# Kernel optimization log

Hardware: AMD Instinct MI355X
Metric: run time of the kernel (lower is better)

Reference implementation:

```python
import jax, jax.numpy as jnp
import numpy as np

B, N, M = 64, 1024, 80
C1, D = 288, 256  # object_dim, lang_dim
EPS = 1e-12  # F.normalize eps


def setup_inputs() -> dict:
    key = jax.random.key(0)
    ks = jax.random.split(key, 16)
    w = lambda k, s: jax.random.normal(k, s, jnp.float32) * 0.05
    object_feat = jax.random.normal(ks[0], (B, N, C1), jnp.float32)
    lang_feat = jax.random.normal(ks[1], (B, M, D), jnp.float32)
    lang_mask = jax.random.randint(ks[2], (B, M), 0, 2).astype(jnp.int32)
    lang_mask = lang_mask.at[:, 0].set(1)  # ensure >=1 valid token per row
    return {
        "object_feat": object_feat,
        "lang_feat": lang_feat,
        "lang_mask": lang_mask,
        # object_att_fc: Linear(C1,D) -> ReLU -> Linear(D,D)
        "W1": w(ks[3], (C1, D)), "b1": w(ks[4], (D,)),
        "W2": w(ks[5], (D, D)), "b2": w(ks[6], (D,)),
        # atten_fc: Dropout(eval=identity) -> Linear(2D,1)
        "Wa": w(ks[7], (2 * D, 1)), "ba": w(ks[8], (1,)),
        # object_score_fc: Linear(C1,D) -> ReLU -> Linear(D,D)
        "W3": w(ks[9], (C1, D)), "b3": w(ks[10], (D,)),
        "W4": w(ks[11], (D, D)), "b4": w(ks[12], (D,)),
        # score_fc: Dropout(eval=identity) -> Linear(D,1)
        "Ws": w(ks[13], (D, 1)), "bs": w(ks[14], (1,)),
    }


def reference(object_feat, lang_feat, lang_mask, W1, b1, W2, b2, Wa, ba, W3, b3, W4, b4, Ws, bs):
    # object attention features: (B,N,D)
    oa = jnp.maximum(object_feat @ W1 + b1, 0.0) @ W2 + b2
    # additive attention: cat([oa, lang]) @ Wa == oa @ Wa[:D] + lang @ Wa[D:]
    w_o, w_l = Wa[:D, 0], Wa[D:, 0]
    score = (oa @ w_o)[:, :, None] + (lang_feat @ w_l)[:, None, :] + ba[0]  # (B,N,M)
    score = jnp.where(lang_mask[:, None, :] == 0, -jnp.inf, score)
    att = jax.nn.softmax(score, axis=2)  # (B,N,M)
    att_feat = jnp.einsum("bnm,bmd->bnd", att, lang_feat)  # sum(att * lang_att)
    # object score branch
    osc = jnp.maximum(object_feat @ W3 + b3, 0.0) @ W4 + b4  # (B,N,D)
    x = jnp.maximum(att_feat * osc, 0.0)
    # F.normalize over channel dim (dim=2)
    nrm = jnp.sqrt(jnp.sum(x * x, axis=2, keepdims=True))
    x = x / jnp.maximum(nrm, EPS)
    out = x @ Ws + bs  # (B,N,1)
    return jnp.transpose(out, (0, 2, 1))  # (B,1,N)
```

## Files before the change

### kernel.cpp

```cpp
#include <hip/hip_runtime.h>
#include <math.h>
#include <stdint.h>

#define B_  64
#define N_  1024
#define M_  80
#define C1_ 288
#define D_  256
#define EPS_ 1e-12f

typedef _Float16 f16;
typedef _Float16 f16x8 __attribute__((ext_vector_type(8)));
typedef _Float16 f16x4 __attribute__((ext_vector_type(4)));
typedef float    f32x4 __attribute__((ext_vector_type(4)));

#define ATT_OFF 0
#define W3F_OFF 65536
#define W4F_OFF (65536 + 147456)

__global__ __launch_bounds__(256) void prep_kernel(
    const float* __restrict__ lang_feat,
    const int*   __restrict__ lang_mask,
    const float* __restrict__ Wa,
    float* __restrict__ att_ws)
{
    __shared__ float wl_s[D_];
    __shared__ float ls[M_];
    const int b   = blockIdx.x;
    const int tid = threadIdx.x;

    wl_s[tid] = Wa[D_ + tid];
    __syncthreads();

    const int wave = tid >> 6, lane = tid & 63;
    for (int m = wave; m < M_; m += 4) {
        const float* lf = lang_feat + (size_t)(b * M_ + m) * D_;
        float p = 0.f;
        #pragma unroll
        for (int j = 0; j < 4; ++j) { int d = lane + 64 * j; p = fmaf(lf[d], wl_s[d], p); }
        #pragma unroll
        for (int off = 32; off; off >>= 1) p += __shfl_xor(p, off);
        if (lane == 0) ls[m] = (lang_mask[b * M_ + m] == 0) ? -INFINITY : p;
    }
    __syncthreads();

    float mx = -INFINITY;
    for (int m = 0; m < M_; ++m) mx = fmaxf(mx, ls[m]);
    __syncthreads();
    if (tid < M_) ls[tid] = expf(ls[tid] - mx);
    __syncthreads();

    float sm = 0.f;
    for (int m = 0; m < M_; ++m) sm += ls[m];

    const int d = tid;
    float acc = 0.f;
    for (int m = 0; m < M_; ++m)
        acc = fmaf(ls[m], lang_feat[(size_t)(b * M_ + m) * D_ + d], acc);
    att_ws[b * D_ + d] = acc / sm;
}

__global__ __launch_bounds__(256) void wprep_kernel(
    const float* __restrict__ W3, const float* __restrict__ W4,
    f16* __restrict__ w3f, f16* __restrict__ w4f)
{
    const int kb = blockIdx.x;
    const float* src; f16* dst; int K0;
    if (kb < 9) { src = W3; dst = w3f + kb * 8192;      K0 = kb * 32; }
    else        { src = W4; dst = w4f + (kb - 9) * 8192; K0 = (kb - 9) * 32; }
    for (int idx = threadIdx.x; idx < 8192; idx += 256) {
        int nt  = idx >> 9;
        int rem = idx & 511;
        int ln  = rem >> 3;
        int i   = rem & 7;
        int k   = K0 + ((ln >> 4) << 3) + i;
        int col = (nt << 4) + (ln & 15);
        dst[idx] = (f16)src[k * D_ + col];
    }
}

__device__ __forceinline__ void g2l16(const void* g, void* l) {
    __builtin_amdgcn_global_load_lds(
        (const __attribute__((address_space(1))) uint32_t*)g,
        (__attribute__((address_space(3))) uint32_t*)l, 16, 0, 0);
}

#define ABYTES 36864
#define BBUF   16384

__global__ __launch_bounds__(512) void main_kernel(
    const float* __restrict__ obj,
    const f16*  __restrict__ w3f,
    const f16*  __restrict__ w4f,
    const float* __restrict__ b3,
    const float* __restrict__ b4,
    const float* __restrict__ Ws,
    const float* __restrict__ bs,
    const float* __restrict__ att,
    float* __restrict__ out)
{
    extern __shared__ char smem[];
    char* Areg = smem;
    char* Breg = smem + ABYTES;

    const int tid  = threadIdx.x;
    const int lane = tid & 63;
    const int w    = tid >> 6;
    const int mt   = w & 3;
    const int ng   = w >> 2;
    const int r0   = blockIdx.x * 64;
    const int b    = blockIdx.x >> 4;

    {
        const float4* src = (const float4*)(obj + (size_t)r0 * C1_);
        for (int idx = tid; idx < 64 * 72; idx += 512) {
            int row = idx / 72;
            int c   = (idx - row * 72) * 4;
            float4 v = src[idx];
            int plane = (row >> 4) * 9 + (c >> 5);
            int lane2 = (row & 15) + (((c & 31) >> 3) << 4);
            int ii    = c & 7;
            f16x4 h = { (f16)v.x, (f16)v.y, (f16)v.z, (f16)v.w };
            *(f16x4*)&Areg[plane * 1024 + lane2 * 16 + ii * 2] = h;
        }
    }

    const int colbase = (ng << 7) + (lane & 15);

    f32x4 acc[8];
    #pragma unroll
    for (int nt = 0; nt < 8; ++nt) {
        float bv = b3[colbase + (nt << 4)];
        acc[nt] = (f32x4){bv, bv, bv, bv};
    }

    {
        const char* g = (const char*)w3f + (w * 2) * 1024 + lane * 16;
        char* l = Breg + (w * 2) * 1024;
        g2l16(g, l); g2l16(g + 1024, l + 1024);
    }
    __syncthreads();

    for (int ks = 0; ks < 9; ++ks) {
        if (ks < 8) {
            const char* g = (const char*)w3f + (ks + 1) * BBUF + (w * 2) * 1024 + lane * 16;
            char* l = Breg + ((ks + 1) & 1) * BBUF + (w * 2) * 1024;
            g2l16(g, l); g2l16(g + 1024, l + 1024);
        }
        f16x8 a = *(const f16x8*)&Areg[(mt * 9 + ks) * 1024 + lane * 16];
        const char* bb = Breg + (ks & 1) * BBUF + (ng << 13);
        #pragma unroll
        for (int nt = 0; nt < 8; ++nt) {
            f16x8 bf = *(const f16x8*)&bb[nt * 1024 + lane * 16];
            acc[nt] = __builtin_amdgcn_mfma_f32_16x16x32_f16(a, bf, acc[nt], 0, 0, 0);
        }
        __syncthreads();
    }

    #pragma unroll
    for (int nt = 0; nt < 8; ++nt) {
        int colg  = colbase + (nt << 4);
        int plane = (mt << 3) + (colg >> 5);
        int l2b   = (((colg & 31) >> 3) << 4);
        int i2    = colg & 7;
        #pragma unroll
        for (int r = 0; r < 4; ++r) {
            int row_l = ((lane >> 4) << 2) + r;
            *(f16*)&Areg[plane * 1024 + (l2b + row_l) * 16 + i2 * 2] = (f16)fmaxf(acc[nt][r], 0.f);
        }
    }

    #pragma unroll
    for (int nt = 0; nt < 8; ++nt) {
        float bv = b4[colbase + (nt << 4)];
        acc[nt] = (f32x4){bv, bv, bv, bv};
    }
    {
        const char* g = (const char*)w4f + (w * 2) * 1024 + lane * 16;
        char* l = Breg + (w * 2) * 1024;
        g2l16(g, l); g2l16(g + 1024, l + 1024);
    }
    __syncthreads();

    for (int ks = 0; ks < 8; ++ks) {
        if (ks < 7) {
            const char* g = (const char*)w4f + (ks + 1) * BBUF + (w * 2) * 1024 + lane * 16;
            char* l = Breg + ((ks + 1) & 1) * BBUF + (w * 2) * 1024;
            g2l16(g, l); g2l16(g + 1024, l + 1024);
        }
        f16x8 a = *(const f16x8*)&Areg[(mt * 8 + ks) * 1024 + lane * 16];
        const char* bb = Breg + (ks & 1) * BBUF + (ng << 13);
        #pragma unroll
        for (int nt = 0; nt < 8; ++nt) {
            f16x8 bf = *(const f16x8*)&bb[nt * 1024 + lane * 16];
            acc[nt] = __builtin_amdgcn_mfma_f32_16x16x32_f16(a, bf, acc[nt], 0, 0, 0);
        }
        __syncthreads();
    }

    const float bsv = bs[0];
    float s2r[4] = {0, 0, 0, 0}, swr[4] = {0, 0, 0, 0};
    #pragma unroll
    for (int nt = 0; nt < 8; ++nt) {
        int colg = colbase + (nt << 4);
        float av = att[(b << 8) + colg];
        float wv = Ws[colg];
        #pragma unroll
        for (int r = 0; r < 4; ++r) {
            float x = fmaxf(av * acc[nt][r], 0.f);
            s2r[r] = fmaf(x, x, s2r[r]);
            swr[r] = fmaf(x, wv, swr[r]);
        }
    }
    #pragma unroll
    for (int off = 1; off < 16; off <<= 1) {
        #pragma unroll
        for (int r = 0; r < 4; ++r) {
            s2r[r] += __shfl_xor(s2r[r], off);
            swr[r] += __shfl_xor(swr[r], off);
        }
    }
    float* red = (float*)Breg;
    if (ng == 0 && (lane & 15) == 0) {
        #pragma unroll
        for (int r = 0; r < 4; ++r) {
            int row = (mt << 4) + ((lane >> 4) << 2) + r;
            red[row * 2]     = s2r[r];
            red[row * 2 + 1] = swr[r];
        }
    }
    __syncthreads();
    if (ng == 1 && (lane & 15) == 0) {
        #pragma unroll
        for (int r = 0; r < 4; ++r) {
            int row = (mt << 4) + ((lane >> 4) << 2) + r;
            float S2 = s2r[r] + red[row * 2];
            float SW = swr[r] + red[row * 2 + 1];
            out[r0 + row] = SW / fmaxf(sqrtf(S2), EPS_) + bsv;
        }
    }
}

extern "C" void kernel_launch(void* const* d_in, const int* in_sizes, int n_in,
                              void* d_out, int out_size, void* d_ws, size_t ws_size,
                              hipStream_t stream) {
    const float* object_feat = (const float*)d_in[0];
    const float* lang_feat   = (const float*)d_in[1];
    const int*   lang_mask   = (const int*)d_in[2];
    const float* Wa = (const float*)d_in[7];
    const float* W3 = (const float*)d_in[9];
    const float* b3 = (const float*)d_in[10];
    const float* W4 = (const float*)d_in[11];
    const float* b4 = (const float*)d_in[12];
    const float* Ws = (const float*)d_in[13];
    const float* bs = (const float*)d_in[14];
    float* out = (float*)d_out;

    char* ws  = (char*)d_ws;
    float* att = (float*)(ws + ATT_OFF);
    f16*  w3f = (f16*)(ws + W3F_OFF);
    f16*  w4f = (f16*)(ws + W4F_OFF);

    prep_kernel<<<B_, 256, 0, stream>>>(lang_feat, lang_mask, Wa, att);
    wprep_kernel<<<17, 256, 0, stream>>>(W3, W4, w3f, w4f);

    main_kernel<<<(B_ * N_) / 64, 512, ABYTES + 2 * BBUF, stream>>>(
        object_feat, w3f, w4f, b3, b4, Ws, bs, att, out);
}
```

Measured before the change: 173.9 us.

## Split fused MLP into two weight-resident GEMM kernels with f16 intermediate

Replaces the single fused kernel, which streamed weights through double-buffered LDS per 64-row tile, with two kernels. Each kernel loads the whole f16 weight matrix into LDS once per block, and each wave computes 32 rows by 256 columns straight from global A loads. The hidden activation h3 is written to workspace as f16, and the two prep kernels are merged into one launch. The cost is an extra global round trip for h3, very large LDS use (144KB and 128KB) that limits occupancy, and heavy register pressure from 32 accumulators per wave.

```diff
diff --git a/kernel.cpp b/kernel.cpp
--- a/kernel.cpp
+++ b/kernel.cpp
@@ -11,22 +11,49 @@
 
 typedef _Float16 f16;
 typedef _Float16 f16x8 __attribute__((ext_vector_type(8)));
-typedef _Float16 f16x4 __attribute__((ext_vector_type(4)));
 typedef float    f32x4 __attribute__((ext_vector_type(4)));
 
 #define ATT_OFF 0
 #define W3F_OFF 65536
 #define W4F_OFF (65536 + 147456)
+#define H3_OFF  (65536 + 147456 + 131072)
+
+__device__ __forceinline__ void g2l16(const void* g, void* l) {
+    __builtin_amdgcn_global_load_lds(
+        (const __attribute__((address_space(1))) uint32_t*)g,
+        (__attribute__((address_space(3))) uint32_t*)l, 16, 0, 0);
+}
 
 __global__ __launch_bounds__(256) void prep_kernel(
     const float* __restrict__ lang_feat,
     const int*   __restrict__ lang_mask,
     const float* __restrict__ Wa,
-    float* __restrict__ att_ws)
+    const float* __restrict__ W3,
+    const float* __restrict__ W4,
+    float* __restrict__ att_ws,
+    f16* __restrict__ w3f, f16* __restrict__ w4f)
 {
+    const int bi = blockIdx.x;
+    if (bi >= B_) {
+        const int kb = bi - B_;
+        const float* src; f16* dst; int K0;
+        if (kb < 9) { src = W3; dst = w3f + kb * 8192;       K0 = kb * 32; }
+        else        { src = W4; dst = w4f + (kb - 9) * 8192; K0 = (kb - 9) * 32; }
+        for (int idx = threadIdx.x; idx < 8192; idx += 256) {
+            int nt  = idx >> 9;
+            int rem = idx & 511;
+            int ln  = rem >> 3;
+            int i   = rem & 7;
+            int k   = K0 + ((ln >> 4) << 3) + i;
+            int col = (nt << 4) + (ln & 15);
+            dst[idx] = (f16)src[k * D_ + col];
+        }
+        return;
+    }
+
     __shared__ float wl_s[D_];
     __shared__ float ls[M_];
-    const int b   = blockIdx.x;
+    const int b   = bi;
     const int tid = threadIdx.x;
 
     wl_s[tid] = Wa[D_ + tid];
@@ -45,54 +72,111 @@
     __syncthreads();
 
     float mx = -INFINITY;
-    for (int m = 0; m < M_; ++m) mx = fmaxf(mx, ls[m]);
+    #pragma unroll
+    for (int m0 = 0; m0 < M_; m0 += 8) {
+        float v0 = ls[m0], v1 = ls[m0+1], v2 = ls[m0+2], v3 = ls[m0+3];
+        float v4 = ls[m0+4], v5 = ls[m0+5], v6 = ls[m0+6], v7 = ls[m0+7];
+        mx = fmaxf(mx, fmaxf(fmaxf(fmaxf(v0,v1), fmaxf(v2,v3)),
+                             fmaxf(fmaxf(v4,v5), fmaxf(v6,v7))));
+    }
     __syncthreads();
     if (tid < M_) ls[tid] = expf(ls[tid] - mx);
     __syncthreads();
 
-    float sm = 0.f;
-    for (int m = 0; m < M_; ++m) sm += ls[m];
+    float s0 = 0.f, s1 = 0.f, s2 = 0.f, s3 = 0.f;
+    #pragma unroll
+    for (int m0 = 0; m0 < M_; m0 += 8) {
+        s0 += ls[m0] + ls[m0+4];
+        s1 += ls[m0+1] + ls[m0+5];
+        s2 += ls[m0+2] + ls[m0+6];
+        s3 += ls[m0+3] + ls[m0+7];
+    }
+    const float inv = 1.f / ((s0 + s1) + (s2 + s3));
 
     const int d = tid;
-    float acc = 0.f;
-    for (int m = 0; m < M_; ++m)
-        acc = fmaf(ls[m], lang_feat[(size_t)(b * M_ + m) * D_ + d], acc);
-    att_ws[b * D_ + d] = acc / sm;
-}
-
-__global__ __launch_bounds__(256) void wprep_kernel(
-    const float* __restrict__ W3, const float* __restrict__ W4,
-    f16* __restrict__ w3f, f16* __restrict__ w4f)
-{
-    const int kb = blockIdx.x;
-    const float* src; f16* dst; int K0;
-    if (kb < 9) { src = W3; dst = w3f + kb * 8192;      K0 = kb * 32; }
-    else        { src = W4; dst = w4f + (kb - 9) * 8192; K0 = (kb - 9) * 32; }
-    for (int idx = threadIdx.x; idx < 8192; idx += 256) {
-        int nt  = idx >> 9;
-        int rem = idx & 511;
-        int ln  = rem >> 3;
-        int i   = rem & 7;
-        int k   = K0 + ((ln >> 4) << 3) + i;
-        int col = (nt << 4) + (ln & 15);
-        dst[idx] = (f16)src[k * D_ + col];
-    }
-}
-
-__device__ __forceinline__ void g2l16(const void* g, void* l) {
-    __builtin_amdgcn_global_load_lds(
-        (const __attribute__((address_space(1))) uint32_t*)g,
-        (__attribute__((address_space(3))) uint32_t*)l, 16, 0, 0);
-}
-
-#define ABYTES 36864
-#define BBUF   16384
-
-__global__ __launch_bounds__(512) void main_kernel(
+    float a0 = 0.f, a1 = 0.f, a2 = 0.f, a3 = 0.f;
+    const float* lfb = lang_feat + (size_t)b * M_ * D_ + d;
+    #pragma unroll 5
+    for (int m = 0; m < M_; m += 4) {
+        a0 = fmaf(ls[m],   lfb[(size_t)m * D_],       a0);
+        a1 = fmaf(ls[m+1], lfb[(size_t)(m+1) * D_],   a1);
+        a2 = fmaf(ls[m+2], lfb[(size_t)(m+2) * D_],   a2);
+        a3 = fmaf(ls[m+3], lfb[(size_t)(m+3) * D_],   a3);
+    }
+    att_ws[b * D_ + d] = ((a0 + a1) + (a2 + a3)) * inv;
+}
+
+__global__ __launch_bounds__(512, 2) void gemm1_kernel(
     const float* __restrict__ obj,
     const f16*  __restrict__ w3f,
+    const float* __restrict__ b3,
+    f16* __restrict__ h3)
+{
+    extern __shared__ char smem[];
+    const int tid  = threadIdx.x;
+    const int lane = tid & 63;
+    const int w    = tid >> 6;
+
+    #pragma unroll
+    for (int i = 0; i < 18; ++i) {
+        int off = (i * 512 + tid) * 16;
+        g2l16((const char*)w3f + off, smem + off);
+    }
+    __syncthreads();
+
+    const int r0   = (blockIdx.x * 8 + w) * 32;
+    const int colc = lane & 15;
+    const int kc   = (lane >> 4) << 3;
+
+    f32x4 acc0[16], acc1[16];
+    #pragma unroll
+    for (int nt = 0; nt < 16; ++nt) {
+        float bv = b3[(nt << 4) + colc];
+        acc0[nt] = (f32x4){bv, bv, bv, bv};
+        acc1[nt] = acc0[nt];
+    }
+
+    const float* arow0 = obj + (size_t)(r0 + colc) * C1_ + kc;
+    const float* arow1 = arow0 + 16 * C1_;
+
+    #pragma unroll 3
+    for (int ks = 0; ks < 9; ++ks) {
+        float4 p00 = *(const float4*)(arow0 + ks * 32);
+        float4 p01 = *(const float4*)(arow0 + ks * 32 + 4);
+        float4 p10 = *(const float4*)(arow1 + ks * 32);
+        float4 p11 = *(const float4*)(arow1 + ks * 32 + 4);
+        f16x8 a0 = {(f16)p00.x,(f16)p00.y,(f16)p00.z,(f16)p00.w,
+                    (f16)p01.x,(f16)p01.y,(f16)p01.z,(f16)p01.w};
+        f16x8 a1 = {(f16)p10.x,(f16)p10.y,(f16)p10.z,(f16)p10.w,
+                    (f16)p11.x,(f16)p11.y,(f16)p11.z,(f16)p11.w};
+        const char* bb = smem + ks * 16384;
+        #pragma unroll
+        for (int nt = 0; nt < 16; ++nt) {
+            f16x8 bf = *(const f16x8*)&bb[nt * 1024 + lane * 16];
+            acc0[nt] = __builtin_amdgcn_mfma_f32_16x16x32_f16(a0, bf, acc0[nt], 0, 0, 0);
+            acc1[nt] = __builtin_amdgcn_mfma_f32_16x16x32_f16(a1, bf, acc1[nt], 0, 0, 0);
+        }
+    }
+
+    const int rbase = (lane >> 4) << 2;
+    #pragma unroll
+    for (int h = 0; h < 2; ++h) {
+        #pragma unroll
+        for (int r = 0; r < 4; ++r) {
+            int row = r0 + 16 * h + rbase + r;
+            f16* dst = h3 + (size_t)row * D_ + colc;
+            #pragma unroll
+            for (int nt = 0; nt < 16; ++nt) {
+                f32x4 a = h ? acc1[nt] : acc0[nt];
+                dst[nt << 4] = (f16)fmaxf(a[r], 0.f);
+            }
+        }
+    }
+}
+
+__global__ __launch_bounds__(512, 2) void gemm2_kernel(
+    const f16*  __restrict__ h3,
     const f16*  __restrict__ w4f,
-    const float* __restrict__ b3,
     const float* __restrict__ b4,
     const float* __restrict__ Ws,
     const float* __restrict__ bs,
@@ -100,143 +184,76 @@
     float* __restrict__ out)
 {
     extern __shared__ char smem[];
-    char* Areg = smem;
-    char* Breg = smem + ABYTES;
-
     const int tid  = threadIdx.x;
     const int lane = tid & 63;
     const int w    = tid >> 6;
-    const int mt   = w & 3;
-    const int ng   = w >> 2;
-    const int r0   = blockIdx.x * 64;
-    const int b    = blockIdx.x >> 4;
-
-    {
-        const float4* src = (const float4*)(obj + (size_t)r0 * C1_);
-        for (int idx = tid; idx < 64 * 72; idx += 512) {
-            int row = idx / 72;
-            int c   = (idx - row * 72) * 4;
-            float4 v = src[idx];
-            int plane = (row >> 4) * 9 + (c >> 5);
-            int lane2 = (row & 15) + (((c & 31) >> 3) << 4);
-            int ii    = c & 7;
-            f16x4 h = { (f16)v.x, (f16)v.y, (f16)v.z, (f16)v.w };
-            *(f16x4*)&Areg[plane * 1024 + lane2 * 16 + ii * 2] = h;
-        }
-    }
-
-    const int colbase = (ng << 7) + (lane & 15);
-
-    f32x4 acc[8];
-    #pragma unroll
-    for (int nt = 0; nt < 8; ++nt) {
-        float bv = b3[colbase + (nt << 4)];
-        acc[nt] = (f32x4){bv, bv, bv, bv};
-    }
-
-    {
-        const char* g = (const char*)w3f + (w * 2) * 1024 + lane * 16;
-        char* l = Breg + (w * 2) * 1024;
-        g2l16(g, l); g2l16(g + 1024, l + 1024);
-    }
-    __syncthreads();
-
-    for (int ks = 0; ks < 9; ++ks) {
-        if (ks < 8) {
-            const char* g = (const char*)w3f + (ks + 1) * BBUF + (w * 2) * 1024 + lane * 16;
-            char* l = Breg + ((ks + 1) & 1) * BBUF + (w * 2) * 1024;
-            g2l16(g, l); g2l16(g + 1024, l + 1024);
-        }
-        f16x8 a = *(const f16x8*)&Areg[(mt * 9 + ks) * 1024 + lane * 16];
-        const char* bb = Breg + (ks & 1) * BBUF + (ng << 13);
-        #pragma unroll
-        for (int nt = 0; nt < 8; ++nt) {
+
+    #pragma unroll
+    for (int i = 0; i < 16; ++i) {
+        int off = (i * 512 + tid) * 16;
+        g2l16((const char*)w4f + off, smem + off);
+    }
+    __syncthreads();
+
+    const int r0   = (blockIdx.x * 8 + w) * 32;
+    const int b    = r0 >> 10;
+    const int colc = lane & 15;
+    const int kcB  = (lane >> 4) << 3;
+
+    f32x4 acc0[16], acc1[16];
+    #pragma unroll
+    for (int nt = 0; nt < 16; ++nt) {
+        float bv = b4[(nt << 4) + colc];
+        acc0[nt] = (f32x4){bv, bv, bv, bv};
+        acc1[nt] = acc0[nt];
+    }
+
+    const f16* a0p = h3 + (size_t)(r0 + colc) * D_ + kcB;
+    const f16* a1p = a0p + 16 * D_;
+
+    #pragma unroll 4
+    for (int ks = 0; ks < 8; ++ks) {
+        f16x8 a0 = *(const f16x8*)(a0p + ks * 32);
+        f16x8 a1 = *(const f16x8*)(a1p + ks * 32);
+        const char* bb = smem + ks * 16384;
+        #pragma unroll
+        for (int nt = 0; nt < 16; ++nt) {
             f16x8 bf = *(const f16x8*)&bb[nt * 1024 + lane * 16];
-            acc[nt] = __builtin_amdgcn_mfma_f32_16x16x32_f16(a, bf, acc[nt], 0, 0, 0);
-        }
-        __syncthreads();
-    }
-
-    #pragma unroll
-    for (int nt = 0; nt < 8; ++nt) {
-        int colg  = colbase + (nt << 4);
-        int plane = (mt << 3) + (colg >> 5);
-        int l2b   = (((colg & 31) >> 3) << 4);
-        int i2    = colg & 7;
-        #pragma unroll
-        for (int r = 0; r < 4; ++r) {
-            int row_l = ((lane >> 4) << 2) + r;
-            *(f16*)&Areg[plane * 1024 + (l2b + row_l) * 16 + i2 * 2] = (f16)fmaxf(acc[nt][r], 0.f);
-        }
-    }
-
-    #pragma unroll
-    for (int nt = 0; nt < 8; ++nt) {
-        float bv = b4[colbase + (nt << 4)];
-        acc[nt] = (f32x4){bv, bv, bv, bv};
-    }
-    {
-        const char* g = (const char*)w4f + (w * 2) * 1024 + lane * 16;
-        char* l = Breg + (w * 2) * 1024;
-        g2l16(g, l); g2l16(g + 1024, l + 1024);
-    }
-    __syncthreads();
-
-    for (int ks = 0; ks < 8; ++ks) {
-        if (ks < 7) {
-            const char* g = (const char*)w4f + (ks + 1) * BBUF + (w * 2) * 1024 + lane * 16;
-            char* l = Breg + ((ks + 1) & 1) * BBUF + (w * 2) * 1024;
-            g2l16(g, l); g2l16(g + 1024, l + 1024);
-        }
-        f16x8 a = *(const f16x8*)&Areg[(mt * 8 + ks) * 1024 + lane * 16];
-        const char* bb = Breg + (ks & 1) * BBUF + (ng << 13);
-        #pragma unroll
-        for (int nt = 0; nt < 8; ++nt) {
-            f16x8 bf = *(const f16x8*)&bb[nt * 1024 + lane * 16];
-            acc[nt] = __builtin_amdgcn_mfma_f32_16x16x32_f16(a, bf, acc[nt], 0, 0, 0);
-        }
-        __syncthreads();
+            acc0[nt] = __builtin_amdgcn_mfma_f32_16x16x32_f16(a0, bf, acc0[nt], 0, 0, 0);
+            acc1[nt] = __builtin_amdgcn_mfma_f32_16x16x32_f16(a1, bf, acc1[nt], 0, 0, 0);
+        }
     }
 
     const float bsv = bs[0];
-    float s2r[4] = {0, 0, 0, 0}, swr[4] = {0, 0, 0, 0};
-    #pragma unroll
-    for (int nt = 0; nt < 8; ++nt) {
-        int colg = colbase + (nt << 4);
+    float s20[4] = {0,0,0,0}, sw0[4] = {0,0,0,0};
+    float s21[4] = {0,0,0,0}, sw1[4] = {0,0,0,0};
+    #pragma unroll
+    for (int nt = 0; nt < 16; ++nt) {
+        int colg = (nt << 4) + colc;
         float av = att[(b << 8) + colg];
         float wv = Ws[colg];
         #pragma unroll
         for (int r = 0; r < 4; ++r) {
-            float x = fmaxf(av * acc[nt][r], 0.f);
-            s2r[r] = fmaf(x, x, s2r[r]);
-            swr[r] = fmaf(x, wv, swr[r]);
+            float x0 = fmaxf(av * acc0[nt][r], 0.f);
+            float x1 = fmaxf(av * acc1[nt][r], 0.f);
+            s20[r] = fmaf(x0, x0, s20[r]);  sw0[r] = fmaf(x0, wv, sw0[r]);
+            s21[r] = fmaf(x1, x1, s21[r]);  sw1[r] = fmaf(x1, wv, sw1[r]);
         }
     }
     #pragma unroll
     for (int off = 1; off < 16; off <<= 1) {
         #pragma unroll
         for (int r = 0; r < 4; ++r) {
-            s2r[r] += __shfl_xor(s2r[r], off);
-            swr[r] += __shfl_xor(swr[r], off);
-        }
-    }
-    float* red = (float*)Breg;
-    if (ng == 0 && (lane & 15) == 0) {
-        #pragma unroll
-        for (int r = 0; r < 4; ++r) {
-            int row = (mt << 4) + ((lane >> 4) << 2) + r;
-            red[row * 2]     = s2r[r];
-            red[row * 2 + 1] = swr[r];
-        }
-    }
-    __syncthreads();
-    if (ng == 1 && (lane & 15) == 0) {
-        #pragma unroll
-        for (int r = 0; r < 4; ++r) {
-            int row = (mt << 4) + ((lane >> 4) << 2) + r;
-            float S2 = s2r[r] + red[row * 2];
-            float SW = swr[r] + red[row * 2 + 1];
-            out[r0 + row] = SW / fmaxf(sqrtf(S2), EPS_) + bsv;
+            s20[r] += __shfl_xor(s20[r], off);  sw0[r] += __shfl_xor(sw0[r], off);
+            s21[r] += __shfl_xor(s21[r], off);  sw1[r] += __shfl_xor(sw1[r], off);
+        }
+    }
+    if (colc == 0) {
+        const int rbase = (lane >> 4) << 2;
+        #pragma unroll
+        for (int r = 0; r < 4; ++r) {
+            out[r0 + rbase + r]      = sw0[r] / fmaxf(sqrtf(s20[r]), EPS_) + bsv;
+            out[r0 + 16 + rbase + r] = sw1[r] / fmaxf(sqrtf(s21[r]), EPS_) + bsv;
         }
     }
 }
@@ -256,14 +273,19 @@
     const float* bs = (const float*)d_in[14];
     float* out = (float*)d_out;
 
-    char* ws  = (char*)d_ws;
+    char* ws   = (char*)d_ws;
     float* att = (float*)(ws + ATT_OFF);
-    f16*  w3f = (f16*)(ws + W3F_OFF);
-    f16*  w4f = (f16*)(ws + W4F_OFF);
-
-    prep_kernel<<<B_, 256, 0, stream>>>(lang_feat, lang_mask, Wa, att);
-    wprep_kernel<<<17, 256, 0, stream>>>(W3, W4, w3f, w4f);
-
-    main_kernel<<<(B_ * N_) / 64, 512, ABYTES + 2 * BBUF, stream>>>(
-        object_feat, w3f, w4f, b3, b4, Ws, bs, att, out);
-}
+    f16*  w3f  = (f16*)(ws + W3F_OFF);
+    f16*  w4f  = (f16*)(ws + W4F_OFF);
+    f16*  h3   = (f16*)(ws + H3_OFF);
+
+    hipFuncSetAttribute(reinterpret_cast<const void*>(gemm1_kernel),
+                        hipFuncAttributeMaxDynamicSharedMemorySize, 147456);
+    hipFuncSetAttribute(reinterpret_cast<const void*>(gemm2_kernel),
+                        hipFuncAttributeMaxDynamicSharedMemorySize, 131072);
+
+    prep_kernel<<<B_ + 17, 256, 0, stream>>>(lang_feat, lang_mask, Wa, W3, W4,
+                                             att, w3f, w4f);
+    gemm1_kernel<<<256, 512, 147456, stream>>>(object_feat, w3f, b3, h3);
+    gemm2_kernel<<<256, 512, 131072, stream>>>(h3, w4f, b4, Ws, bs, att, out);
+}
```

Result: no change. 171.6 us (-1.3%).
